# Performance work log

Hardware: AMD Instinct MI355X
Metric: run time of the kernel (lower is better)

## Reference

```python
import jax, jax.numpy as jnp
import numpy as np

NUM_EMBEDDINGS = 1024
EMBEDDING_DIM = 64
COMMITMENT_COST = 0.25


def setup_inputs() -> dict:
    key = jax.random.key(0)
    k1, k2 = jax.random.split(key)
    z_e = jax.random.normal(k1, (32, 64, 64, 64), dtype=jnp.float32)  # NHWC
    lim = 1.0 / NUM_EMBEDDINGS
    embeddings = jax.random.uniform(
        k2, (NUM_EMBEDDINGS, EMBEDDING_DIM), minval=-lim, maxval=lim, dtype=jnp.float32
    )
    return {"z_e": z_e, "embeddings": embeddings}


def reference(z_e, embeddings):
    D = embeddings.shape[1]
    # Faithful to the TF module: NHWC -> NCHW, then flatten into rows of length D.
    z = jnp.transpose(z_e, (0, 3, 1, 2))            # [B, C, H, W]
    flat = z.reshape(-1, D)                          # [N, D]
    # Squared distances via GEMM (argmin of ||.||^2 == argmin of ||.||); avoids the [N, K, D] tensor.
    d2 = (
        jnp.sum(flat * flat, axis=-1, keepdims=True)
        - 2.0 * flat @ embeddings.T
        + jnp.sum(embeddings * embeddings, axis=-1)
    )                                                # [N, K]
    indices = jnp.argmin(d2, axis=1)                 # [N]
    z_q = embeddings[indices].reshape(z.shape)       # [B, C, H, W]
    z_q_st = z_q + jax.lax.stop_gradient(z - z_q)    # straight-through estimator
    e_latent_loss = jnp.mean((jax.lax.stop_gradient(z_q) - z) ** 2)
    q_latent_loss = jnp.mean((z_q_st - jax.lax.stop_gradient(z)) ** 2)
    loss = q_latent_loss + COMMITMENT_COST * e_latent_loss
    return jnp.transpose(z_q_st, (0, 2, 3, 1)), indices, loss
```

## Files before the change

### kernel.cpp

```cpp
#include <hip/hip_runtime.h>


#define N_Z 8388608
#define N_IDX 131072
#define K_EMB 1024
#define D_EMB 64
#define EPS_GAP 7e-5f

__global__ __launch_bounds__(256) void ek2f_kernel(
    const float* __restrict__ emb, float* __restrict__ ek2f) {
  int k = blockIdx.x * 256 + threadIdx.x;
  const float* row = emb + (size_t)k * D_EMB;
  float s = 0.0f;
  for (int d = 0; d < D_EMB; d++) {
    float e = row[d];
    float sq = e * e;
    asm volatile("" : "+v"(sq));
    s = s + sq;
  }
  ek2f[k] = s;
}

__global__ __launch_bounds__(256) void vq_main_kernel(
    const float* __restrict__ z, const float* __restrict__ emb,
    const float* __restrict__ ek2g, float* __restrict__ out_idx,
    double* __restrict__ loss_acc) {
  __shared__ __align__(16) float zts[64][64];
  __shared__ __align__(16) float et2[64][64];
  __shared__ float sk2[K_EMB];
  __shared__ float sa[64];
  __shared__ int sidx[64];
  __shared__ int sflag[64];
  __shared__ double lred[16];
  __shared__ float wrv[4];
  __shared__ int wri[4];

  const int t = threadIdx.x;
  const int bid = blockIdx.x;
  const int j = t & 15;
  const int i4 = t >> 4;

  const float4* zt4 = (const float4*)(z + (size_t)bid * 4096);
  #pragma unroll
  for (int q = 0; q < 4; q++) {
    int p = t + q * 256;
    float4 v = zt4[p];
    int w = p >> 4;
    int c = (p & 15) * 4;
    *(float4*)&zts[w][c] = v;
  }
  #pragma unroll
  for (int q = 0; q < 4; q++) sk2[t + q * 256] = ek2g[t + q * 256];
  __syncthreads();

  if (t < 64) {
    float a = 0.0f;
    for (int w = 0; w < 64; w++) {
      float zf = zts[w][t];
      float sq = zf * zf;
      asm volatile("" : "+v"(sq));
      a = a + sq;
    }
    sa[t] = a;
  }
  __syncthreads();

  float A_[4];
  #pragma unroll
  for (int ci = 0; ci < 4; ci++) A_[ci] = sa[i4 * 4 + ci];

  float m1[4], m2[4];
  int i1[4];
  #pragma unroll
  for (int ci = 0; ci < 4; ci++) { m1[ci] = 3.0e38f; m2[ci] = 3.0e38f; i1[ci] = 0; }

  for (int kt = 0; kt < 16; kt++) {
    __syncthreads();
    {
      int k = t & 63;
      int w4b = t >> 6;
      int col = (k & 15) * 4 + (k >> 4);
      #pragma unroll
      for (int q = 0; q < 4; q++) {
        int w4 = w4b + q * 4;
        float4 v = *(const float4*)(emb + (size_t)(kt * 64 + k) * 64 + w4 * 4);
        et2[w4 * 4 + 0][col] = v.x; et2[w4 * 4 + 1][col] = v.y;
        et2[w4 * 4 + 2][col] = v.z; et2[w4 * 4 + 3][col] = v.w;
      }
    }
    __syncthreads();

    float acc[4][4];
    #pragma unroll
    for (int ci = 0; ci < 4; ci++)
      #pragma unroll
      for (int s = 0; s < 4; s++) acc[ci][s] = 0.0f;

    #pragma unroll 8
    for (int w = 0; w < 64; w++) {
      float4 zr = *(const float4*)&zts[w][i4 * 4];
      float4 er = *(const float4*)&et2[w][j * 4];
      acc[0][0] += zr.x * er.x; acc[0][1] += zr.x * er.y;
      acc[0][2] += zr.x * er.z; acc[0][3] += zr.x * er.w;
      acc[1][0] += zr.y * er.x; acc[1][1] += zr.y * er.y;
      acc[1][2] += zr.y * er.z; acc[1][3] += zr.y * er.w;
      acc[2][0] += zr.z * er.x; acc[2][1] += zr.z * er.y;
      acc[2][2] += zr.z * er.z; acc[2][3] += zr.z * er.w;
      acc[3][0] += zr.w * er.x; acc[3][1] += zr.w * er.y;
      acc[3][2] += zr.w * er.z; acc[3][3] += zr.w * er.w;
    }

    #pragma unroll
    for (int s = 0; s < 4; s++) {
      int k = kt * 64 + j + 16 * s;
      float ck = sk2[k];
      #pragma unroll
      for (int ci = 0; ci < 4; ci++) {
        float sc = fmaf(-2.0f, acc[ci][s], A_[ci]) + ck;
        if (sc < m1[ci]) { m2[ci] = m1[ci]; m1[ci] = sc; i1[ci] = k; }
        else             { m2[ci] = fminf(m2[ci], sc); }
      }
    }
  }

  #pragma unroll
  for (int ci = 0; ci < 4; ci++) {
    float v1 = m1[ci], v2 = m2[ci];
    int ix = i1[ci];
    #pragma unroll
    for (int m = 8; m; m >>= 1) {
      float ov1 = __shfl_xor(v1, m, 16);
      int oi1 = __shfl_xor(ix, m, 16);
      float ov2 = __shfl_xor(v2, m, 16);
      if (ov1 < v1)      { v2 = fminf(v1, ov2); v1 = ov1; ix = oi1; }
      else if (ov1 > v1) { v2 = fminf(v2, ov1); }
      else               { v2 = v1; ix = min(ix, oi1); }
    }
    m1[ci] = v1; m2[ci] = v2; i1[ci] = ix;
  }
  if (j == 0) {
    #pragma unroll
    for (int ci = 0; ci < 4; ci++) {
      int c = i4 * 4 + ci;
      sidx[c] = i1[ci];
      sflag[c] = (m2[ci] - m1[ci] <= EPS_GAP) ? 1 : 0;
    }
  }
  __syncthreads();

  for (int c = 0; c < 64; c++) {
    if (!sflag[c]) continue;
    float A = sa[c];
    float lm = 3.0e38f;
    int li = 0;
    #pragma unroll
    for (int r = 0; r < 4; r++) {
      int k = t + 256 * r;
      double B = 0.0;
      const float4* e4 = (const float4*)(emb + (size_t)k * 64);
      for (int w4 = 0; w4 < 16; w4++) {
        float4 e = e4[w4];
        B += (double)zts[w4 * 4 + 0][c] * (double)e.x;
        B += (double)zts[w4 * 4 + 1][c] * (double)e.y;
        B += (double)zts[w4 * 4 + 2][c] * (double)e.z;
        B += (double)zts[w4 * 4 + 3][c] * (double)e.w;
      }
      float Bf = (float)B;
      float t1 = A - 2.0f * Bf;
      float sc = t1 + sk2[k];
      if (sc < lm) { lm = sc; li = k; }
    }
    #pragma unroll
    for (int m = 32; m; m >>= 1) {
      float ov = __shfl_xor(lm, m);
      int oi = __shfl_xor(li, m);
      if (ov < lm || (ov == lm && oi < li)) { lm = ov; li = oi; }
    }
    int wid = t >> 6;
    if ((t & 63) == 0) { wrv[wid] = lm; wri[wid] = li; }
    __syncthreads();
    if (t == 0) {
      float bv = wrv[0]; int bi = wri[0];
      #pragma unroll
      for (int q = 1; q < 4; q++) {
        if (wrv[q] < bv || (wrv[q] == bv && wri[q] < bi)) { bv = wrv[q]; bi = wri[q]; }
      }
      sidx[c] = bi;
    }
    __syncthreads();
  }
  __syncthreads();

  const int b = bid >> 6, h = bid & 63;
  if (t < 64) out_idx[(size_t)b * 4096 + t * 64 + h] = (float)sidx[t];

  double ls = 0.0;
  #pragma unroll
  for (int ci = 0; ci < 4; ci++) {
    int c = i4 * 4 + ci;
    const float* er = emb + (size_t)sidx[c] * 64;
    #pragma unroll
    for (int s = 0; s < 4; s++) {
      int w = j + 16 * s;
      double d = (double)zts[w][c] - (double)er[w];
      ls += d * d;
    }
  }
  #pragma unroll
  for (int m = 8; m; m >>= 1) ls += __shfl_xor(ls, m, 16);
  if (j == 0) lred[i4] = ls;
  __syncthreads();
  if (t == 0) {
    double s = 0.0;
    #pragma unroll
    for (int q = 0; q < 16; q++) s += lred[q];
    atomicAdd(loss_acc, s);
  }
}

__global__ void loss_final_kernel(const double* __restrict__ acc,
                                  float* __restrict__ out_loss) {
  *out_loss = (float)(0.25 * (*acc) / (double)N_Z);
}

extern "C" void kernel_launch(void* const* d_in, const int* in_sizes, int n_in,
                              void* d_out, int out_size, void* d_ws, size_t ws_size,
                              hipStream_t stream) {
  const float* z = (const float*)d_in[0];
  const float* emb = (const float*)d_in[1];
  float* out = (float*)d_out;

  float* ek2f = (float*)d_ws;
  double* lacc = (double*)((char*)d_ws + 4096);

  (void)hipMemsetAsync(lacc, 0, sizeof(double), stream);
  (void)hipMemcpyAsync(out, z, (size_t)N_Z * sizeof(float),
                       hipMemcpyDeviceToDevice, stream);
  ek2f_kernel<<<4, 256, 0, stream>>>(emb, ek2f);
  vq_main_kernel<<<2048, 256, 0, stream>>>(z, emb, ek2f, out + N_Z, lacc);
  loss_final_kernel<<<1, 1, 0, stream>>>(lacc, out + N_Z + N_IDX);
}
```

Baseline: 467.2 us.

## Double-buffer codebook tiles with register prefetch in VQ main loop

Codebook tiles move to a two-slot shared-memory buffer. The next tile is loaded into registers before the current tile's dot-product loop and written to the alternate slot afterward, which cuts the loop from two barriers per iteration to one. The aim is to hide global-load latency behind the FMA work. In exchange it doubles the LDS used for the tile and adds 16 live registers, which could lower occupancy.

```diff
diff --git a/kernel.cpp b/kernel.cpp
--- a/kernel.cpp
+++ b/kernel.cpp
@@ -26,7 +26,7 @@
     const float* __restrict__ ek2g, float* __restrict__ out_idx,
     double* __restrict__ loss_acc) {
   __shared__ __align__(16) float zts[64][64];
-  __shared__ __align__(16) float et2[64][64];
+  __shared__ __align__(16) float et2[2][64][64];
   __shared__ float sk2[K_EMB];
   __shared__ float sa[64];
   __shared__ int sidx[64];
@@ -40,17 +40,29 @@
   const int j = t & 15;
   const int i4 = t >> 4;
 
+  const int kk = t & 63;
+  const int w4b = t >> 6;
+  const int col = (kk & 15) * 4 + (kk >> 4);
+
   const float4* zt4 = (const float4*)(z + (size_t)bid * 4096);
+  float4 pf[4];
+  #pragma unroll
+  for (int q = 0; q < 4; q++)
+    pf[q] = *(const float4*)(emb + (size_t)kk * 64 + (w4b + q * 4) * 4);
   #pragma unroll
   for (int q = 0; q < 4; q++) {
     int p = t + q * 256;
     float4 v = zt4[p];
-    int w = p >> 4;
-    int c = (p & 15) * 4;
-    *(float4*)&zts[w][c] = v;
+    *(float4*)&zts[p >> 4][(p & 15) * 4] = v;
   }
   #pragma unroll
   for (int q = 0; q < 4; q++) sk2[t + q * 256] = ek2g[t + q * 256];
+  #pragma unroll
+  for (int q = 0; q < 4; q++) {
+    int w4 = w4b + q * 4;
+    et2[0][w4 * 4 + 0][col] = pf[q].x; et2[0][w4 * 4 + 1][col] = pf[q].y;
+    et2[0][w4 * 4 + 2][col] = pf[q].z; et2[0][w4 * 4 + 3][col] = pf[q].w;
+  }
   __syncthreads();
 
   if (t < 64) {
@@ -75,20 +87,13 @@
   for (int ci = 0; ci < 4; ci++) { m1[ci] = 3.0e38f; m2[ci] = 3.0e38f; i1[ci] = 0; }
 
   for (int kt = 0; kt < 16; kt++) {
-    __syncthreads();
-    {
-      int k = t & 63;
-      int w4b = t >> 6;
-      int col = (k & 15) * 4 + (k >> 4);
-      #pragma unroll
-      for (int q = 0; q < 4; q++) {
-        int w4 = w4b + q * 4;
-        float4 v = *(const float4*)(emb + (size_t)(kt * 64 + k) * 64 + w4 * 4);
-        et2[w4 * 4 + 0][col] = v.x; et2[w4 * 4 + 1][col] = v.y;
-        et2[w4 * 4 + 2][col] = v.z; et2[w4 * 4 + 3][col] = v.w;
-      }
-    }
-    __syncthreads();
+    const int cur = kt & 1;
+    if (kt < 15) {
+      const float* src = emb + (size_t)((kt + 1) * 64 + kk) * 64;
+      #pragma unroll
+      for (int q = 0; q < 4; q++)
+        pf[q] = *(const float4*)(src + (w4b + q * 4) * 4);
+    }
 
     float acc[4][4];
     #pragma unroll
@@ -99,7 +104,7 @@
     #pragma unroll 8
     for (int w = 0; w < 64; w++) {
       float4 zr = *(const float4*)&zts[w][i4 * 4];
-      float4 er = *(const float4*)&et2[w][j * 4];
+      float4 er = *(const float4*)&et2[cur][w][j * 4];
       acc[0][0] += zr.x * er.x; acc[0][1] += zr.x * er.y;
       acc[0][2] += zr.x * er.z; acc[0][3] += zr.x * er.w;
       acc[1][0] += zr.y * er.x; acc[1][1] += zr.y * er.y;
@@ -121,6 +126,18 @@
         else             { m2[ci] = fminf(m2[ci], sc); }
       }
     }
+
+    if (kt < 15) {
+      #pragma unroll
+      for (int q = 0; q < 4; q++) {
+        int w4 = w4b + q * 4;
+        et2[cur ^ 1][w4 * 4 + 0][col] = pf[q].x;
+        et2[cur ^ 1][w4 * 4 + 1][col] = pf[q].y;
+        et2[cur ^ 1][w4 * 4 + 2][col] = pf[q].z;
+        et2[cur ^ 1][w4 * 4 + 3][col] = pf[q].w;
+      }
+    }
+    __syncthreads();
   }
 
   #pragma unroll
```

Result: slower. 486.0 us (+4.0%).

## Compute distance GEMM with split-bf16 MFMA and double-buffered codebook tiles

Applied to the files above, without the earlier changes.

Replaces the scalar FP32 dot-product loop with bf16 MFMA instructions, splitting both z and the codebook into hi/lo bf16 parts (three-term product) to approximate FP32 accuracy. A prep kernel pre-swizzles the codebook into an MFMA-friendly bf16 layout, and the main kernel double-buffers codebook chunks in LDS with register prefetch, so each chunk needs one barrier instead of two. The near-tie threshold is widened so the FP64 fallback rescoring catches the extra rounding error, at the cost of possibly more rows taking that slow path.

```diff
diff --git a/kernel.cpp b/kernel.cpp
--- a/kernel.cpp
+++ b/kernel.cpp
@@ -5,7 +5,19 @@
 #define N_IDX 131072
 #define K_EMB 1024
 #define D_EMB 64
-#define EPS_GAP 7e-5f
+#define EPS_GAP 1.25e-4f
+
+typedef __attribute__((ext_vector_type(8))) short bf16x8;
+typedef __attribute__((ext_vector_type(4))) float f32x4;
+
+__device__ __forceinline__ unsigned short f2bf(float f) {
+  unsigned u = __builtin_bit_cast(unsigned, f);
+  unsigned r = 0x7fffu + ((u >> 16) & 1u);
+  return (unsigned short)((u + r) >> 16);
+}
+__device__ __forceinline__ float bf2f(unsigned short b) {
+  return __builtin_bit_cast(float, (unsigned)b << 16);
+}
 
 __global__ __launch_bounds__(256) void ek2f_kernel(
     const float* __restrict__ emb, float* __restrict__ ek2f) {
@@ -21,12 +33,36 @@
   ek2f[k] = s;
 }
 
+__global__ __launch_bounds__(256) void ebf_prep_kernel(
+    const float* __restrict__ emb, unsigned short* __restrict__ ehi,
+    unsigned short* __restrict__ elo) {
+  int gid = blockIdx.x * 256 + threadIdx.x;
+  int k = gid >> 3, oct = gid & 7;
+  const float* src = emb + (size_t)k * 64 + oct * 8;
+  int kt = k >> 4, sp = oct >> 2, l = (oct & 3) * 16 + (k & 15);
+  size_t off = ((size_t)((kt * 2 + sp) * 64 + l)) * 8;
+  bf16x8 h8, l8;
+  #pragma unroll
+  for (int i = 0; i < 8; i++) {
+    float v = src[i];
+    unsigned short hb = f2bf(v);
+    float lf = v - bf2f(hb);
+    h8[i] = (short)hb;
+    l8[i] = (short)f2bf(lf);
+  }
+  *(bf16x8*)(ehi + off) = h8;
+  *(bf16x8*)(elo + off) = l8;
+}
+
 __global__ __launch_bounds__(256) void vq_main_kernel(
     const float* __restrict__ z, const float* __restrict__ emb,
-    const float* __restrict__ ek2g, float* __restrict__ out_idx,
-    double* __restrict__ loss_acc) {
+    const float* __restrict__ ek2g,
+    const unsigned short* __restrict__ ehi_g,
+    const unsigned short* __restrict__ elo_g,
+    float* __restrict__ out_idx, double* __restrict__ loss_acc) {
   __shared__ __align__(16) float zts[64][64];
-  __shared__ __align__(16) float et2[64][64];
+  __shared__ __align__(16) unsigned short lhi[2][4096];
+  __shared__ __align__(16) unsigned short llo[2][4096];
   __shared__ float sk2[K_EMB];
   __shared__ float sa[64];
   __shared__ int sidx[64];
@@ -37,20 +73,27 @@
 
   const int t = threadIdx.x;
   const int bid = blockIdx.x;
-  const int j = t & 15;
-  const int i4 = t >> 4;
+  const int l = t & 63;
+  const int wv = t >> 6;
+  const int cb = wv * 16;
 
   const float4* zt4 = (const float4*)(z + (size_t)bid * 4096);
   #pragma unroll
   for (int q = 0; q < 4; q++) {
     int p = t + q * 256;
     float4 v = zt4[p];
-    int w = p >> 4;
-    int c = (p & 15) * 4;
-    *(float4*)&zts[w][c] = v;
+    *(float4*)&zts[p >> 4][(p & 15) * 4] = v;
   }
   #pragma unroll
   for (int q = 0; q < 4; q++) sk2[t + q * 256] = ek2g[t + q * 256];
+  {
+    const int tt = t & 127;
+    const uint4* src = (t < 128) ? (const uint4*)ehi_g : (const uint4*)elo_g;
+    unsigned short* dst = (t < 128) ? lhi[0] : llo[0];
+    #pragma unroll
+    for (int q = 0; q < 4; q++)
+      *(uint4*)&dst[tt * 32 + q * 8] = src[tt * 4 + q];
+  }
   __syncthreads();
 
   if (t < 64) {
@@ -63,64 +106,78 @@
     }
     sa[t] = a;
   }
+
+  bf16x8 zh0, zh1, zl0, zl1;
+  {
+    const int crow = cb + (l & 15);
+    const int wb = (l >> 4) * 8;
+    #pragma unroll
+    for (int i = 0; i < 8; i++) {
+      float zf = zts[wb + i][crow];
+      unsigned short hb = f2bf(zf);
+      float lf = zf - bf2f(hb);
+      zh0[i] = (short)hb; zl0[i] = (short)f2bf(lf);
+      float zf1 = zts[32 + wb + i][crow];
+      unsigned short hb1 = f2bf(zf1);
+      float lf1 = zf1 - bf2f(hb1);
+      zh1[i] = (short)hb1; zl1[i] = (short)f2bf(lf1);
+    }
+  }
   __syncthreads();
 
   float A_[4];
   #pragma unroll
-  for (int ci = 0; ci < 4; ci++) A_[ci] = sa[i4 * 4 + ci];
+  for (int i = 0; i < 4; i++) A_[i] = sa[cb + ((l >> 4) & 3) * 4 + i];
 
   float m1[4], m2[4];
   int i1[4];
   #pragma unroll
-  for (int ci = 0; ci < 4; ci++) { m1[ci] = 3.0e38f; m2[ci] = 3.0e38f; i1[ci] = 0; }
-
-  for (int kt = 0; kt < 16; kt++) {
+  for (int i = 0; i < 4; i++) { m1[i] = 3.0e38f; m2[i] = 3.0e38f; i1[i] = 0; }
+
+  for (int ch = 0; ch < 16; ch++) {
+    const int cur = ch & 1;
+    uint4 pf[4];
+    if (ch < 15) {
+      const int tt = t & 127;
+      const uint4* src = (t < 128) ? (const uint4*)ehi_g : (const uint4*)elo_g;
+      #pragma unroll
+      for (int q = 0; q < 4; q++)
+        pf[q] = src[(size_t)(ch + 1) * 512 + tt * 4 + q];
+    }
+
+    #pragma unroll
+    for (int t4 = 0; t4 < 4; t4++) {
+      const int fb = (t4 * 2) * 64 * 8 + l * 8;
+      bf16x8 bh0 = *(const bf16x8*)&lhi[cur][fb];
+      bf16x8 bh1 = *(const bf16x8*)&lhi[cur][fb + 512];
+      bf16x8 bl0 = *(const bf16x8*)&llo[cur][fb];
+      bf16x8 bl1 = *(const bf16x8*)&llo[cur][fb + 512];
+      f32x4 acc = {0.f, 0.f, 0.f, 0.f};
+      acc = __builtin_amdgcn_mfma_f32_16x16x32_bf16(zh0, bh0, acc, 0, 0, 0);
+      acc = __builtin_amdgcn_mfma_f32_16x16x32_bf16(zh1, bh1, acc, 0, 0, 0);
+      acc = __builtin_amdgcn_mfma_f32_16x16x32_bf16(zh0, bl0, acc, 0, 0, 0);
+      acc = __builtin_amdgcn_mfma_f32_16x16x32_bf16(zh1, bl1, acc, 0, 0, 0);
+      acc = __builtin_amdgcn_mfma_f32_16x16x32_bf16(zl0, bh0, acc, 0, 0, 0);
+      acc = __builtin_amdgcn_mfma_f32_16x16x32_bf16(zl1, bh1, acc, 0, 0, 0);
+
+      const int k = ch * 64 + t4 * 16 + (l & 15);
+      const float ck = sk2[k];
+      #pragma unroll
+      for (int i = 0; i < 4; i++) {
+        float sc = fmaf(-2.0f, acc[i], A_[i]) + ck;
+        if (sc < m1[i]) { m2[i] = m1[i]; m1[i] = sc; i1[i] = k; }
+        else            { m2[i] = fminf(m2[i], sc); }
+      }
+    }
+
+    if (ch < 15) {
+      const int tt = t & 127;
+      unsigned short* dst = (t < 128) ? lhi[cur ^ 1] : llo[cur ^ 1];
+      #pragma unroll
+      for (int q = 0; q < 4; q++)
+        *(uint4*)&dst[tt * 32 + q * 8] = pf[q];
+    }
     __syncthreads();
-    {
-      int k = t & 63;
-      int w4b = t >> 6;
-      int col = (k & 15) * 4 + (k >> 4);
-      #pragma unroll
-      for (int q = 0; q < 4; q++) {
-        int w4 = w4b + q * 4;
-        float4 v = *(const float4*)(emb + (size_t)(kt * 64 + k) * 64 + w4 * 4);
-        et2[w4 * 4 + 0][col] = v.x; et2[w4 * 4 + 1][col] = v.y;
-        et2[w4 * 4 + 2][col] = v.z; et2[w4 * 4 + 3][col] = v.w;
-      }
-    }
-    __syncthreads();
-
-    float acc[4][4];
-    #pragma unroll
-    for (int ci = 0; ci < 4; ci++)
-      #pragma unroll
-      for (int s = 0; s < 4; s++) acc[ci][s] = 0.0f;
-
-    #pragma unroll 8
-    for (int w = 0; w < 64; w++) {
-      float4 zr = *(const float4*)&zts[w][i4 * 4];
-      float4 er = *(const float4*)&et2[w][j * 4];
-      acc[0][0] += zr.x * er.x; acc[0][1] += zr.x * er.y;
-      acc[0][2] += zr.x * er.z; acc[0][3] += zr.x * er.w;
-      acc[1][0] += zr.y * er.x; acc[1][1] += zr.y * er.y;
-      acc[1][2] += zr.y * er.z; acc[1][3] += zr.y * er.w;
-      acc[2][0] += zr.z * er.x; acc[2][1] += zr.z * er.y;
-      acc[2][2] += zr.z * er.z; acc[2][3] += zr.z * er.w;
-      acc[3][0] += zr.w * er.x; acc[3][1] += zr.w * er.y;
-      acc[3][2] += zr.w * er.z; acc[3][3] += zr.w * er.w;
-    }
-
-    #pragma unroll
-    for (int s = 0; s < 4; s++) {
-      int k = kt * 64 + j + 16 * s;
-      float ck = sk2[k];
-      #pragma unroll
-      for (int ci = 0; ci < 4; ci++) {
-        float sc = fmaf(-2.0f, acc[ci][s], A_[ci]) + ck;
-        if (sc < m1[ci]) { m2[ci] = m1[ci]; m1[ci] = sc; i1[ci] = k; }
-        else             { m2[ci] = fminf(m2[ci], sc); }
-      }
-    }
   }
 
   #pragma unroll
@@ -138,10 +195,10 @@
     }
     m1[ci] = v1; m2[ci] = v2; i1[ci] = ix;
   }
-  if (j == 0) {
+  if ((t & 15) == 0) {
     #pragma unroll
     for (int ci = 0; ci < 4; ci++) {
-      int c = i4 * 4 + ci;
+      int c = (t >> 4) * 4 + ci;
       sidx[c] = i1[ci];
       sflag[c] = (m2[ci] - m1[ci] <= EPS_GAP) ? 1 : 0;
     }
@@ -176,8 +233,7 @@
       int oi = __shfl_xor(li, m);
       if (ov < lm || (ov == lm && oi < li)) { lm = ov; li = oi; }
     }
-    int wid = t >> 6;
-    if ((t & 63) == 0) { wrv[wid] = lm; wri[wid] = li; }
+    if ((t & 63) == 0) { wrv[t >> 6] = lm; wri[t >> 6] = li; }
     __syncthreads();
     if (t == 0) {
       float bv = wrv[0]; int bi = wri[0];
@@ -197,18 +253,18 @@
   double ls = 0.0;
   #pragma unroll
   for (int ci = 0; ci < 4; ci++) {
-    int c = i4 * 4 + ci;
+    int c = (t >> 4) * 4 + ci;
     const float* er = emb + (size_t)sidx[c] * 64;
     #pragma unroll
     for (int s = 0; s < 4; s++) {
-      int w = j + 16 * s;
+      int w = (t & 15) + 16 * s;
       double d = (double)zts[w][c] - (double)er[w];
       ls += d * d;
     }
   }
   #pragma unroll
   for (int m = 8; m; m >>= 1) ls += __shfl_xor(ls, m, 16);
-  if (j == 0) lred[i4] = ls;
+  if ((t & 15) == 0) lred[t >> 4] = ls;
   __syncthreads();
   if (t == 0) {
     double s = 0.0;
@@ -232,11 +288,15 @@
 
   float* ek2f = (float*)d_ws;
   double* lacc = (double*)((char*)d_ws + 4096);
+  unsigned short* ehi = (unsigned short*)((char*)d_ws + 8192);
+  unsigned short* elo = (unsigned short*)((char*)d_ws + 8192 + 131072);
 
   (void)hipMemsetAsync(lacc, 0, sizeof(double), stream);
   (void)hipMemcpyAsync(out, z, (size_t)N_Z * sizeof(float),
                        hipMemcpyDeviceToDevice, stream);
   ek2f_kernel<<<4, 256, 0, stream>>>(emb, ek2f);
-  vq_main_kernel<<<2048, 256, 0, stream>>>(z, emb, ek2f, out + N_Z, lacc);
+  ebf_prep_kernel<<<32, 256, 0, stream>>>(emb, ehi, elo);
+  vq_main_kernel<<<2048, 256, 0, stream>>>(z, emb, ek2f, ehi, elo,
+                                           out + N_Z, lacc);
   loss_final_kernel<<<1, 1, 0, stream>>>(lacc, out + N_Z + N_IDX);
 }
```

Result: faster. 447.9 us (-4.1%).
